# Kernel optimization log

Measured on AMD Instinct MI355X. Metric: run time of the kernel, lower is better.

The kernel has to match this reference:

```python
import jax, jax.numpy as jnp
import numpy as np
from jax import lax

EPS = 1e-5

def conv2d(x, w, pad):
    # x: NCHW, w: OIHW
    return lax.conv_general_dilated(x, w, (1, 1), [(pad, pad), (pad, pad)],
                                    dimension_numbers=('NCHW', 'OIHW', 'NCHW'))

def batchnorm(x, gamma, beta):
    # training-mode BN: batch statistics over N,H,W (biased variance, as torch)
    m = jnp.mean(x, axis=(0, 2, 3), keepdims=True)
    v = jnp.var(x, axis=(0, 2, 3), keepdims=True)
    g = gamma.reshape(1, -1, 1, 1)
    b = beta.reshape(1, -1, 1, 1)
    return (x - m) * jax.lax.rsqrt(v + EPS) * g + b

def setup_inputs() -> dict:
    key = jax.random.key(0)
    ks = jax.random.split(key, 8)
    B, Cin, Cmid, NC, H, W = 4, 2048, 512, 19, 64, 64
    s = lambda fan: (2.0 / fan) ** 0.5
    return {
        'x':  jax.random.normal(ks[0], (B, Cin, H, W), jnp.float32),
        'Wa': jax.random.normal(ks[1], (Cmid, Cin, 3, 3), jnp.float32) * s(Cin * 9),
        'ga': jnp.ones((Cmid,), jnp.float32),
        'ba': jnp.zeros((Cmid,), jnp.float32),
        'Wb': jax.random.normal(ks[2], (Cmid, Cmid, 1, 1), jnp.float32) * s(Cmid),
        'bb': jnp.zeros((Cmid,), jnp.float32),
        'W1': jax.random.normal(ks[3], (Cmid, Cin + Cmid, 3, 3), jnp.float32) * s((Cin + Cmid) * 9),
        'g1': jnp.ones((Cmid,), jnp.float32),
        'b1': jnp.zeros((Cmid,), jnp.float32),
        'W4': jax.random.normal(ks[4], (NC, Cmid, 1, 1), jnp.float32) * s(Cmid),
        'b4': jnp.zeros((NC,), jnp.float32),
    }

def reference(x, Wa, ga, ba, Wb, bb, W1, g1, b1, W4, b4):
    # conva: 3x3 conv (no bias) -> BN -> ReLU
    out = jax.nn.relu(batchnorm(conv2d(x, Wa, 1), ga, ba))
    # convb: 1x1 conv with bias
    out = conv2d(out, Wb, 0) + bb.reshape(1, -1, 1, 1)
    # concat input with projected features along channels
    out = jnp.concatenate([x, out], axis=1)  # [B, Cin+Cmid, H, W]
    # b1 (3x3, no bias) -> b2 BN -> b3 ReLU
    out = jax.nn.relu(batchnorm(conv2d(out, W1, 1), g1, b1))
    # b4: 1x1 classifier conv with bias
    out_final = conv2d(out, W4, 0) + b4.reshape(1, -1, 1, 1)
    return (out, out_final)
```

## Files before the change

kernel.cpp:

```cpp
#include <hip/hip_runtime.h>

typedef unsigned short ushort_t;
typedef unsigned int uint_t;
typedef unsigned long long ulong_t;

typedef __bf16 bf16x8 __attribute__((ext_vector_type(8)));
typedef float f32x4 __attribute__((ext_vector_type(4)));
typedef unsigned short u16x4 __attribute__((ext_vector_type(4)));

#define DEV __device__ __forceinline__
#define SB() __builtin_amdgcn_sched_barrier(0)
#define WAITV(n) asm volatile("s_waitcnt vmcnt(" #n ")" ::: "memory")

DEV ushort_t f2bf(float x) {
  uint_t u = __float_as_uint(x);
  u += 0x7fffu + ((u >> 16) & 1u);
  return (ushort_t)(u >> 16);
}
DEV float bf2f(ushort_t h) { return __uint_as_float(((uint_t)h) << 16); }

DEV void gload16(ulong_t g, const ushort_t* l) {
  __builtin_amdgcn_global_load_lds(
      (__attribute__((address_space(1))) void*)g,
      (__attribute__((address_space(3))) void*)(ushort_t*)l,
      16, 0, 0);
}
DEV int nxt3(int x) { return x == 2 ? 0 : x + 1; }

__global__ void zero_k(float* __restrict__ p, int n) {
  int i = blockIdx.x * 256 + threadIdx.x;
  if (i < n) p[i] = 0.f;
}

__global__ __launch_bounds__(256) void cvt_x_k(const float* __restrict__ X,
                                               ushort_t* __restrict__ P) {
  __shared__ float T[64][65];
  const int t = threadIdx.x;
  const int p0 = blockIdx.x * 64;
  const int c0 = blockIdx.y * 64;
  const int b = p0 >> 12;
  const int pin0 = p0 & 4095;
#pragma unroll
  for (int it = 0; it < 4; ++it) {
    const int cl = it * 16 + (t >> 4);
    const int pl = (t & 15) * 4;
    const f32x4 v = *(const f32x4*)&X[((size_t)(b * 2048 + c0 + cl)) * 4096 + pin0 + pl];
#pragma unroll
    for (int j = 0; j < 4; ++j) T[cl][pl + j] = v[j];
  }
  __syncthreads();
#pragma unroll
  for (int it = 0; it < 4; ++it) {
    const int pl = it * 16 + (t >> 4);
    const int cl = (t & 15) * 4;
    u16x4 h, l;
#pragma unroll
    for (int j = 0; j < 4; ++j) {
      float v = T[cl + j][pl];
      ushort_t hh = f2bf(v);
      h[j] = hh;
      l[j] = f2bf(v - bf2f(hh));
    }
    const int c = c0 + cl;
    const size_t o = (size_t)(p0 + pl) * 4096 + (size_t)((c >> 5) << 6) + (c & 31);
    *(u16x4*)&P[o] = h;
    *(u16x4*)&P[o + 32] = l;
  }
}

__global__ __launch_bounds__(256) void cvt_w3_k(const float* __restrict__ W,
                                                ushort_t* __restrict__ P,
                                                int I, int O) {
  const int t = threadIdx.x;
  const int o = blockIdx.y;
  const int i = blockIdx.x * 256 + t;
  const float* src = W + ((size_t)o * I + i) * 9;
  float v[9];
#pragma unroll
  for (int j = 0; j < 9; ++j) v[j] = src[j];
#pragma unroll
  for (int j = 0; j < 9; ++j) {
    ushort_t h = f2bf(v[j]);
    const size_t d = (size_t)(j * O + o) * (I * 2) + (size_t)((i >> 5) << 6) + (i & 31);
    P[d] = h;
    P[d + 32] = f2bf(v[j] - bf2f(h));
  }
}

__global__ __launch_bounds__(256) void cvt_e_k(const float* __restrict__ W,
                                               ushort_t* __restrict__ P) {
  int i = blockIdx.x * 256 + threadIdx.x;
  float v = W[i];
  ushort_t h = f2bf(v);
  const int o = i >> 9, ic = i & 511;
  const size_t d = (size_t)o * 1024 + (size_t)((ic >> 5) << 6) + (ic & 31);
  P[d] = h;
  P[d + 32] = f2bf(v - bf2f(h));
}

__global__ __launch_bounds__(256) void stats_k(const float* __restrict__ X,
                                               float* __restrict__ S,
                                               float* __restrict__ Q) {
  const int t = threadIdx.x;
  const int r0 = blockIdx.x * 32;
  const int c = t * 2;
  float s0 = 0, s1 = 0, q0 = 0, q1 = 0;
  for (int r = 0; r < 32; ++r) {
    const float2 v = *(const float2*)&X[((size_t)(r0 + r)) * 512 + c];
    s0 += v.x; s1 += v.y;
    q0 += v.x * v.x; q1 += v.y * v.y;
  }
  atomicAdd(&S[c], s0); atomicAdd(&S[c + 1], s1);
  atomicAdd(&Q[c], q0); atomicAdd(&Q[c + 1], q1);
}

__global__ void bnparams_k(const float* __restrict__ S, const float* __restrict__ Q,
                           const float* __restrict__ g, const float* __restrict__ b,
                           float* __restrict__ sc, float* __restrict__ sh) {
  const int t = threadIdx.x;
  const float m = S[t] * (1.0f / 16384.0f);
  const float v = Q[t] * (1.0f / 16384.0f) - m * m;
  const float inv = rsqrtf(v + 1e-5f);
  const float s = g[t] * inv;
  sc[t] = s;
  sh[t] = b[t] - m * s;
}

__global__ __launch_bounds__(256) void bnact_k(const float* __restrict__ X,
                                               const float* __restrict__ sc,
                                               const float* __restrict__ sh,
                                               ushort_t* __restrict__ P) {
  const size_t i0 = ((size_t)blockIdx.x * 256 + threadIdx.x) * 16;
  const int c0 = (int)(i0 & 511);
  const size_t px = i0 >> 9;
#pragma unroll
  for (int q = 0; q < 4; ++q) {
    const f32x4 v = *(const f32x4*)&X[i0 + q * 4];
    const f32x4 s = *(const f32x4*)&sc[c0 + q * 4];
    const f32x4 d = *(const f32x4*)&sh[c0 + q * 4];
    u16x4 h, l;
#pragma unroll
    for (int j = 0; j < 4; ++j) {
      float y = fmaf(v[j], s[j], d[j]);
      y = fmaxf(y, 0.f);
      ushort_t hh = f2bf(y);
      h[j] = hh;
      l[j] = f2bf(y - bf2f(hh));
    }
    const int c = c0 + q * 4;
    const size_t o = px * 1024 + (size_t)((c >> 5) << 6) + (c & 31);
    *(u16x4*)&P[o] = h;
    *(u16x4*)&P[o + 32] = l;
  }
}

__global__ __launch_bounds__(256) void bn_nchw_k(const float* __restrict__ X,
                                                 const float* __restrict__ sc,
                                                 const float* __restrict__ sh,
                                                 float* __restrict__ O) {
  __shared__ float T[64][65];
  const int t = threadIdx.x;
  const int p0 = blockIdx.x * 64;
  const int c0 = blockIdx.y * 64;
  const int b = p0 >> 12, pin0 = p0 & 4095;
#pragma unroll
  for (int it = 0; it < 4; ++it) {
    const int pl = it * 16 + (t >> 4);
    const int cl = (t & 15) * 4;
    const f32x4 v = *(const f32x4*)&X[((size_t)(p0 + pl)) * 512 + c0 + cl];
#pragma unroll
    for (int j = 0; j < 4; ++j) {
      float y = fmaf(v[j], sc[c0 + cl + j], sh[c0 + cl + j]);
      T[pl][cl + j] = fmaxf(y, 0.f);
    }
  }
  __syncthreads();
#pragma unroll
  for (int it = 0; it < 4; ++it) {
    const int cl = it * 16 + (t >> 4);
    const int pl = (t & 15) * 4;
    f32x4 o;
#pragma unroll
    for (int j = 0; j < 4; ++j) o[j] = T[pl + j][cl];
    *(f32x4*)&O[((size_t)(b * 512 + c0 + cl)) * 4096 + pin0 + pl] = o;
  }
}

__global__ __launch_bounds__(256) void conv4_k(const float* __restrict__ X,
                                               const float* __restrict__ sc,
                                               const float* __restrict__ sh,
                                               const float* __restrict__ W4,
                                               const float* __restrict__ B4,
                                               float* __restrict__ O) {
  __shared__ float A[256][69];
  __shared__ float WL[64][19];
  const int t = threadIdx.x;
  const int g0 = blockIdx.x * 256;
  float acc[19];
#pragma unroll
  for (int n = 0; n < 19; ++n) acc[n] = 0.f;
  for (int kc = 0; kc < 8; ++kc) {
    const int k0 = kc * 64;
    __syncthreads();
#pragma unroll
    for (int it = 0; it < 16; ++it) {
      const int rl = it * 16 + (t >> 4);
      const int cl = (t & 15) * 4;
      const f32x4 v = *(const f32x4*)&X[((size_t)(g0 + rl)) * 512 + k0 + cl];
#pragma unroll
      for (int j = 0; j < 4; ++j)
        A[rl][cl + j] = fmaxf(fmaf(v[j], sc[k0 + cl + j], sh[k0 + cl + j]), 0.f);
    }
    for (int e = t; e < 1216; e += 256) {
      int k = e / 19, n = e - k * 19;
      WL[k][n] = W4[(size_t)n * 512 + k0 + k];
    }
    __syncthreads();
#pragma unroll 8
    for (int k = 0; k < 64; ++k) {
      const float a = A[t][k];
#pragma unroll
      for (int n = 0; n < 19; ++n) acc[n] = fmaf(a, WL[k][n], acc[n]);
    }
  }
  const int g = g0 + t;
  const int b = g >> 12, pin = g & 4095;
#pragma unroll
  for (int n = 0; n < 19; ++n)
    O[((size_t)(b * 19 + n)) * 4096 + pin] = acc[n] + B4[n];
}

template <int TAPS, int EPI>
__global__ __launch_bounds__(512, 1) void conv_k(
    const ushort_t* __restrict__ A1, int S1, int CB1,
    const ushort_t* __restrict__ A2, int S2, int CB2,
    const ushort_t* __restrict__ WB, int CBt,
    const ushort_t* __restrict__ zp,
    float* __restrict__ Co, ushort_t* __restrict__ Cp,
    const float* __restrict__ bias) {
  constexpr int RW = (TAPS == 9) ? 6 : 4;
  constexpr int AJ = RW * 4;
  constexpr int AI = (2 * AJ) / 8;
  constexpr int APL = AJ * 1024;
  constexpr int ABUF = 2 * APL;
  constexpr int HO = (TAPS == 9) ? 64 : 0;
  __shared__ ushort_t Alds[49152];
  __shared__ ushort_t Blds[24576];
  const int t = threadIdx.x, lane = t & 63, wid = t >> 6;
  const int wr = wid >> 1, wc = wid & 1;
  const int gid = blockIdx.x, xcd = gid & 7, k_ = gid >> 3;
  const int by = xcd * 8 + (k_ & 7), bx = k_ >> 3;
  const int b = by >> 4, r0 = (by & 15) * 4, bbase = b * 4096;
  const int gsrcA = ((lane & 3) - ((lane >> 3) & 3)) & 3;
  const int NBS = CBt * 64;

  auto stageA = [&](int cb, int bufA) {
#pragma unroll
    for (int i = 0; i < AI; ++i) {
      const int idx = wid * AI + i;
      const int d = idx / AJ, j = idx - d * AJ;
      const int irow = r0 + (j >> 2) - ((TAPS == 9) ? 1 : 0);
      int cbl = cb;
      const ushort_t* base = A1;
      int S = S1;
      if (CB2 > 0 && cbl >= CB1) { base = A2; S = S2; cbl -= CB1; }
      const int gpx = bbase + irow * 64 + (j & 3) * 16 + (lane >> 2);
      const ulong_t el = (ulong_t)gpx * (uint_t)S + (uint_t)(cbl * 64 + d * 32 + gsrcA * 8);
      const bool oob = (unsigned)irow >= 64u;
      const ulong_t src = oob ? (ulong_t)(zp + lane * 8) : (ulong_t)(base + el);
      gload16(src, (const ushort_t*)((const char*)Alds + bufA + (d * AJ + j) * 1024));
    }
  };
  auto stageB = [&](int cb, int tapIdx, int bufB) {
#pragma unroll
    for (int q = 0; q < 2; ++q) {
      const int s = wid * 2 + q, d = s >> 3, nf = s & 7;
      const int cout = bx * 128 + nf * 16 + (lane & 15);
      const ulong_t el = (ulong_t)(tapIdx * 512 + cout) * (uint_t)NBS +
                         (uint_t)(cb * 64 + d * 32 + (lane >> 4) * 8);
      gload16((ulong_t)(WB + el), (const ushort_t*)((const char*)Blds + bufB + s * 1024));
    }
  };

  f32x4 acc[4][4];
#pragma unroll
  for (int i = 0; i < 4; ++i)
#pragma unroll
    for (int j2 = 0; j2 < 4; ++j2) acc[i][j2] = (f32x4){0.f, 0.f, 0.f, 0.f};

  auto compute = [&](int abufB, int bbufB, int ro, int dx) {
    const char* Ab = (const char*)Alds + abufB;
    const char* Bb = (const char*)Blds + bbufB;
    bf16x8 ah[4], al[4], bh[4], bl[4];
#pragma unroll
    for (int i = 0; i < 4; ++i) {
      int px = wr * 64 + i * 16 + (lane & 15) + ro;
      px = px < 0 ? 0 : (px > RW * 64 - 1 ? RW * 64 - 1 : px);
      const int ao = px * 64 + ((((lane >> 4) + (px >> 1)) & 3) * 16);
      ah[i] = *(const bf16x8*)(Ab + ao);
      al[i] = *(const bf16x8*)(Ab + APL + ao);
      bh[i] = *(const bf16x8*)(Bb + (wc * 4 + i) * 1024 + lane * 16);
      bl[i] = *(const bf16x8*)(Bb + 8192 + (wc * 4 + i) * 1024 + lane * 16);
    }
    if (TAPS == 9) {
      if (dx == -1 && (lane & 15) == 0) { bf16x8 z = {}; ah[0] = z; al[0] = z; }
      if (dx == 1 && (lane & 15) == 15) { bf16x8 z = {}; ah[3] = z; al[3] = z; }
    }
    __builtin_amdgcn_s_setprio(1);
#pragma unroll
    for (int mi = 0; mi < 4; ++mi)
#pragma unroll
      for (int ni = 0; ni < 4; ++ni)
        acc[mi][ni] = __builtin_amdgcn_mfma_f32_16x16x32_bf16(ah[mi], bh[ni], acc[mi][ni], 0, 0, 0);
#pragma unroll
    for (int mi = 0; mi < 4; ++mi)
#pragma unroll
      for (int ni = 0; ni < 4; ++ni) {
        acc[mi][ni] = __builtin_amdgcn_mfma_f32_16x16x32_bf16(ah[mi], bl[ni], acc[mi][ni], 0, 0, 0);
        acc[mi][ni] = __builtin_amdgcn_mfma_f32_16x16x32_bf16(al[mi], bh[ni], acc[mi][ni], 0, 0, 0);
      }
    __builtin_amdgcn_s_setprio(0);
  };

  if constexpr (TAPS == 9) {
    int bT = 0;
    stageA(0, 0); SB();
    stageB(0, 0, 0); SB();
    stageB(0, 1, 16384); SB();
    for (int cs = 0; cs < CBt; ++cs) {
      const int abufB = (cs & 1) * ABUF;
#pragma unroll
      for (int tap = 0; tap < 9; ++tap) {
        const int dy = tap / 3 - 1, dx = tap % 3 - 1;
        SB();
        if (tap == 8) { WAITV(8); } else { WAITV(2); }
        SB();
        __builtin_amdgcn_s_barrier();
        SB();
        const int tgt = nxt3(nxt3(bT)) * 16384;
        if (tap < 7) {
          stageB(cs, tap + 2, tgt);
        } else if (tap == 7) {
          stageA(cs + 1, ((cs + 1) & 1) * ABUF);
          stageB(cs + 1, 0, tgt);
        } else {
          stageB(cs + 1, 1, tgt);
        }
        SB();
        compute(abufB, bT * 16384, HO + dy * 64 + dx, dx);
        bT = nxt3(bT);
      }
    }
  } else {
    int rr = 0;
    stageA(0, 0); SB();
    stageB(0, 0, 0); SB();
    stageA(1, ABUF); SB();
    stageB(1, 0, 16384); SB();
    for (int cs = 0; cs < CBt; ++cs) {
      SB();
      WAITV(6);
      SB();
      __builtin_amdgcn_s_barrier();
      SB();
      const int rr2 = nxt3(nxt3(rr));
      stageA(cs + 2, rr2 * ABUF);
      stageB(cs + 2, 0, rr2 * 16384);
      SB();
      compute(rr * ABUF, rr * 16384, 0, 0);
      rr = nxt3(rr);
    }
  }

  const int row0 = by * 256 + wr * 64;
  const int col0 = bx * 128 + wc * 64;
  if (EPI == 0) {
#pragma unroll
    for (int mi = 0; mi < 4; ++mi)
#pragma unroll
      for (int ni = 0; ni < 4; ++ni) {
        const int c = col0 + ni * 16 + (lane & 15);
#pragma unroll
        for (int j2 = 0; j2 < 4; ++j2) {
          const int r = row0 + mi * 16 + (lane >> 4) * 4 + j2;
          Co[(size_t)r * 512 + c] = acc[mi][ni][j2];
        }
      }
  } else {
#pragma unroll
    for (int ni = 0; ni < 4; ++ni) {
      const int c = col0 + ni * 16 + (lane & 15);
      const float bv = bias[c];
      const size_t cg = (size_t)((c >> 5) << 6) + (c & 31);
#pragma unroll
      for (int mi = 0; mi < 4; ++mi)
#pragma unroll
        for (int j2 = 0; j2 < 4; ++j2) {
          const int r = row0 + mi * 16 + (lane >> 4) * 4 + j2;
          const float v = acc[mi][ni][j2] + bv;
          const ushort_t h = f2bf(v);
          Cp[(size_t)r * 1024 + cg] = h;
          Cp[(size_t)r * 1024 + cg + 32] = f2bf(v - bf2f(h));
        }
    }
  }
}

extern "C" void kernel_launch(void* const* d_in, const int* in_sizes, int n_in,
                              void* d_out, int out_size, void* d_ws, size_t ws_size,
                              hipStream_t stream) {
  const float* x  = (const float*)d_in[0];
  const float* Wa = (const float*)d_in[1];
  const float* ga = (const float*)d_in[2];
  const float* ba = (const float*)d_in[3];
  const float* Wb = (const float*)d_in[4];
  const float* bb = (const float*)d_in[5];
  const float* W1 = (const float*)d_in[6];
  const float* g1 = (const float*)d_in[7];
  const float* b1 = (const float*)d_in[8];
  const float* W4 = (const float*)d_in[9];
  const float* b4 = (const float*)d_in[10];
  float* out0 = (float*)d_out;
  float* outF = out0 + (size_t)4 * 512 * 64 * 64;

  char* ws = (char*)d_ws;
  size_t off = 0;
  auto take = [&](size_t bytes) -> char* {
    char* p = ws + off;
    off += (bytes + 255) & ~(size_t)255;
    return p;
  };
  const size_t PAD = 16384;
  ushort_t* zp  = (ushort_t*)take(8192);
  float* sumA = (float*)take(2048);
  float* ssA  = (float*)take(2048);
  float* scA  = (float*)take(2048);
  float* shA  = (float*)take(2048);
  float* sum1 = (float*)take(2048);
  float* ss1  = (float*)take(2048);
  float* sc1  = (float*)take(2048);
  float* sh1  = (float*)take(2048);
  ushort_t* X2  = (ushort_t*)take((size_t)16384 * 4096 * 2 + PAD);
  ushort_t* WA2 = (ushort_t*)take((size_t)9 * 512 * 4096 * 2 + PAD);
  ushort_t* W12 = (ushort_t*)take((size_t)9 * 512 * 5120 * 2 + PAD);
  ushort_t* WBb = (ushort_t*)take((size_t)512 * 1024 * 2 + PAD);
  ushort_t* oA2 = (ushort_t*)take((size_t)16384 * 1024 * 2 + PAD);
  ushort_t* oB2 = (ushort_t*)take((size_t)16384 * 1024 * 2 + PAD);
  float* convaRaw = (float*)take((size_t)16384 * 512 * 4);
  float* conv1Raw = (float*)take((size_t)16384 * 512 * 4);
  if (ws_size < off) return;

  zero_k<<<dim3(24), dim3(256), 0, stream>>>((float*)ws, 6144);
  cvt_x_k<<<dim3(256, 32), dim3(256), 0, stream>>>(x, X2);
  cvt_w3_k<<<dim3(8, 512), dim3(256), 0, stream>>>(Wa, WA2, 2048, 512);
  cvt_w3_k<<<dim3(10, 512), dim3(256), 0, stream>>>(W1, W12, 2560, 512);
  cvt_e_k<<<dim3(1024), dim3(256), 0, stream>>>(Wb, WBb);

  conv_k<9, 0><<<dim3(256), dim3(512), 0, stream>>>(
      X2, 4096, 66, X2, 4096, 0, WA2, 64, zp, convaRaw, nullptr, nullptr);
  stats_k<<<dim3(512), dim3(256), 0, stream>>>(convaRaw, sumA, ssA);
  bnparams_k<<<dim3(1), dim3(512), 0, stream>>>(sumA, ssA, ga, ba, scA, shA);
  bnact_k<<<dim3(2048), dim3(256), 0, stream>>>(convaRaw, scA, shA, oA2);

  conv_k<1, 1><<<dim3(256), dim3(512), 0, stream>>>(
      oA2, 1024, 18, oA2, 1024, 0, WBb, 16, zp, nullptr, oB2, bb);

  conv_k<9, 0><<<dim3(256), dim3(512), 0, stream>>>(
      X2, 4096, 64, oB2, 1024, 16, W12, 80, zp, conv1Raw, nullptr, nullptr);
  stats_k<<<dim3(512), dim3(256), 0, stream>>>(conv1Raw, sum1, ss1);
  bnparams_k<<<dim3(1), dim3(512), 0, stream>>>(sum1, ss1, g1, b1, sc1, sh1);

  bn_nchw_k<<<dim3(256, 8), dim3(256), 0, stream>>>(conv1Raw, sc1, sh1, out0);
  conv4_k<<<dim3(64), dim3(256), 0, stream>>>(conv1Raw, sc1, sh1, W4, b4, outF);
}
```

Before: 2.010 ms.

## Switch conv GEMM to 32x32x16 MFMA with two-tap pipelined staging

Replaces the 16x16x32 bf16 MFMA tiling in the conv kernel with 32x32x16 MFMAs, changing the B-tile LDS layout and swizzle and the epilogue row mapping to match. The 3x3 path now processes two taps per barrier with a four-slot weight ring buffer in a single merged 160KB LDS array. The aim is fewer LDS reads per FLOP and fewer barriers. The full vmcnt drain each step may expose load latency, and launch_bounds is raised to 2 even though the LDS use only allows one block per CU.

```diff
diff --git a/kernel.cpp b/kernel.cpp
--- a/kernel.cpp
+++ b/kernel.cpp
@@ -6,6 +6,7 @@
 
 typedef __bf16 bf16x8 __attribute__((ext_vector_type(8)));
 typedef float f32x4 __attribute__((ext_vector_type(4)));
+typedef float f32x16 __attribute__((ext_vector_type(16)));
 typedef unsigned short u16x4 __attribute__((ext_vector_type(4)));
 
 #define DEV __device__ __forceinline__
@@ -19,10 +20,10 @@
 }
 DEV float bf2f(ushort_t h) { return __uint_as_float(((uint_t)h) << 16); }
 
-DEV void gload16(ulong_t g, const ushort_t* l) {
+DEV void gload16(ulong_t g, const void* l) {
   __builtin_amdgcn_global_load_lds(
       (__attribute__((address_space(1))) void*)g,
-      (__attribute__((address_space(3))) void*)(ushort_t*)l,
+      (__attribute__((address_space(3))) void*)(void*)l,
       16, 0, 0);
 }
 DEV int nxt3(int x) { return x == 2 ? 0 : x + 1; }
@@ -231,7 +232,7 @@
 }
 
 template <int TAPS, int EPI>
-__global__ __launch_bounds__(512, 1) void conv_k(
+__global__ __launch_bounds__(512, 2) void conv_k(
     const ushort_t* __restrict__ A1, int S1, int CB1,
     const ushort_t* __restrict__ A2, int S2, int CB2,
     const ushort_t* __restrict__ WB, int CBt,
@@ -244,14 +245,15 @@
   constexpr int APL = AJ * 1024;
   constexpr int ABUF = 2 * APL;
   constexpr int HO = (TAPS == 9) ? 64 : 0;
-  __shared__ ushort_t Alds[49152];
-  __shared__ ushort_t Blds[24576];
+  __shared__ char lds_all[163840];
+  char* Ald = lds_all;
+  char* Bld = lds_all + 98304;
   const int t = threadIdx.x, lane = t & 63, wid = t >> 6;
   const int wr = wid >> 1, wc = wid & 1;
   const int gid = blockIdx.x, xcd = gid & 7, k_ = gid >> 3;
   const int by = xcd * 8 + (k_ & 7), bx = k_ >> 3;
   const int b = by >> 4, r0 = (by & 15) * 4, bbase = b * 4096;
-  const int gsrcA = ((lane & 3) - ((lane >> 3) & 3)) & 3;
+  const int gsrc = ((lane & 3) - ((lane >> 3) & 3)) & 3;
   const int NBS = CBt * 64;
 
   auto stageA = [&](int cb, int bufA) {
@@ -265,90 +267,124 @@
       int S = S1;
       if (CB2 > 0 && cbl >= CB1) { base = A2; S = S2; cbl -= CB1; }
       const int gpx = bbase + irow * 64 + (j & 3) * 16 + (lane >> 2);
-      const ulong_t el = (ulong_t)gpx * (uint_t)S + (uint_t)(cbl * 64 + d * 32 + gsrcA * 8);
+      const ulong_t el = (ulong_t)gpx * (uint_t)S + (uint_t)(cbl * 64 + d * 32 + gsrc * 8);
       const bool oob = (unsigned)irow >= 64u;
       const ulong_t src = oob ? (ulong_t)(zp + lane * 8) : (ulong_t)(base + el);
-      gload16(src, (const ushort_t*)((const char*)Alds + bufA + (d * AJ + j) * 1024));
+      gload16(src, Ald + bufA + (d * AJ + j) * 1024);
     }
   };
   auto stageB = [&](int cb, int tapIdx, int bufB) {
 #pragma unroll
     for (int q = 0; q < 2; ++q) {
-      const int s = wid * 2 + q, d = s >> 3, nf = s & 7;
-      const int cout = bx * 128 + nf * 16 + (lane & 15);
-      const ulong_t el = (ulong_t)(tapIdx * 512 + cout) * (uint_t)NBS +
-                         (uint_t)(cb * 64 + d * 32 + (lane >> 4) * 8);
-      gload16((ulong_t)(WB + el), (const ushort_t*)((const char*)Blds + bufB + s * 1024));
+      const int s = wid * 2 + q;
+      const int d = s >> 3, r = s & 7, nb = r >> 1, h = r & 1;
+      const int co = bx * 128 + nb * 32 + h * 16 + (lane >> 2);
+      const ulong_t el = (ulong_t)(tapIdx * 512 + co) * (uint_t)NBS +
+                         (uint_t)(cb * 64 + d * 32 + gsrc * 8);
+      gload16((ulong_t)(WB + el), Bld + bufB + s * 1024);
     }
   };
 
-  f32x4 acc[4][4];
-#pragma unroll
-  for (int i = 0; i < 4; ++i)
-#pragma unroll
-    for (int j2 = 0; j2 < 4; ++j2) acc[i][j2] = (f32x4){0.f, 0.f, 0.f, 0.f};
+  f32x16 acc[2][2];
+#pragma unroll
+  for (int i = 0; i < 2; ++i)
+#pragma unroll
+    for (int j2 = 0; j2 < 2; ++j2) acc[i][j2] = (f32x16){0.f};
+
+  const int pxl = lane & 31;
+  const int khalf = lane >> 5;
+  const int rotB = (pxl >> 1) & 3;
+  int boff[2][2];
+#pragma unroll
+  for (int ni = 0; ni < 2; ++ni)
+#pragma unroll
+    for (int kk = 0; kk < 2; ++kk) {
+      const int pos = (kk * 2 + khalf + rotB) & 3;
+      boff[ni][kk] = (wc * 2 + ni) * 2048 + pxl * 64 + pos * 16;
+    }
 
   auto compute = [&](int abufB, int bbufB, int ro, int dx) {
-    const char* Ab = (const char*)Alds + abufB;
-    const char* Bb = (const char*)Blds + bbufB;
-    bf16x8 ah[4], al[4], bh[4], bl[4];
-#pragma unroll
-    for (int i = 0; i < 4; ++i) {
-      int px = wr * 64 + i * 16 + (lane & 15) + ro;
-      px = px < 0 ? 0 : (px > RW * 64 - 1 ? RW * 64 - 1 : px);
-      const int ao = px * 64 + ((((lane >> 4) + (px >> 1)) & 3) * 16);
-      ah[i] = *(const bf16x8*)(Ab + ao);
-      al[i] = *(const bf16x8*)(Ab + APL + ao);
-      bh[i] = *(const bf16x8*)(Bb + (wc * 4 + i) * 1024 + lane * 16);
-      bl[i] = *(const bf16x8*)(Bb + 8192 + (wc * 4 + i) * 1024 + lane * 16);
-    }
+    const char* Ab = Ald + abufB;
+    const char* Bb = Bld + bbufB;
+    bf16x8 a[2][2][2], bf[2][2][2];
+#pragma unroll
+    for (int mi = 0; mi < 2; ++mi)
+#pragma unroll
+      for (int kk = 0; kk < 2; ++kk) {
+        int px = wr * 64 + mi * 32 + pxl + ro;
+        px = px < 0 ? 0 : (px > RW * 64 - 1 ? RW * 64 - 1 : px);
+        const int pos = (kk * 2 + khalf + (px >> 1)) & 3;
+        const int ao = px * 64 + pos * 16;
+        a[mi][kk][0] = *(const bf16x8*)(Ab + ao);
+        a[mi][kk][1] = *(const bf16x8*)(Ab + APL + ao);
+      }
+#pragma unroll
+    for (int ni = 0; ni < 2; ++ni)
+#pragma unroll
+      for (int kk = 0; kk < 2; ++kk) {
+        bf[ni][kk][0] = *(const bf16x8*)(Bb + boff[ni][kk]);
+        bf[ni][kk][1] = *(const bf16x8*)(Bb + 8192 + boff[ni][kk]);
+      }
     if (TAPS == 9) {
-      if (dx == -1 && (lane & 15) == 0) { bf16x8 z = {}; ah[0] = z; al[0] = z; }
-      if (dx == 1 && (lane & 15) == 15) { bf16x8 z = {}; ah[3] = z; al[3] = z; }
+      if (dx == -1 && pxl == 0) {
+        bf16x8 z = {};
+        a[0][0][0] = z; a[0][0][1] = z; a[0][1][0] = z; a[0][1][1] = z;
+      }
+      if (dx == 1 && pxl == 31) {
+        bf16x8 z = {};
+        a[1][0][0] = z; a[1][0][1] = z; a[1][1][0] = z; a[1][1][1] = z;
+      }
     }
     __builtin_amdgcn_s_setprio(1);
 #pragma unroll
-    for (int mi = 0; mi < 4; ++mi)
-#pragma unroll
-      for (int ni = 0; ni < 4; ++ni)
-        acc[mi][ni] = __builtin_amdgcn_mfma_f32_16x16x32_bf16(ah[mi], bh[ni], acc[mi][ni], 0, 0, 0);
-#pragma unroll
-    for (int mi = 0; mi < 4; ++mi)
-#pragma unroll
-      for (int ni = 0; ni < 4; ++ni) {
-        acc[mi][ni] = __builtin_amdgcn_mfma_f32_16x16x32_bf16(ah[mi], bl[ni], acc[mi][ni], 0, 0, 0);
-        acc[mi][ni] = __builtin_amdgcn_mfma_f32_16x16x32_bf16(al[mi], bh[ni], acc[mi][ni], 0, 0, 0);
-      }
+    for (int kk = 0; kk < 2; ++kk)
+#pragma unroll
+      for (int mi = 0; mi < 2; ++mi)
+#pragma unroll
+        for (int ni = 0; ni < 2; ++ni) {
+          acc[mi][ni] = __builtin_amdgcn_mfma_f32_32x32x16_bf16(
+              a[mi][kk][0], bf[ni][kk][0], acc[mi][ni], 0, 0, 0);
+          acc[mi][ni] = __builtin_amdgcn_mfma_f32_32x32x16_bf16(
+              a[mi][kk][0], bf[ni][kk][1], acc[mi][ni], 0, 0, 0);
+          acc[mi][ni] = __builtin_amdgcn_mfma_f32_32x32x16_bf16(
+              a[mi][kk][1], bf[ni][kk][0], acc[mi][ni], 0, 0, 0);
+        }
     __builtin_amdgcn_s_setprio(0);
   };
 
   if constexpr (TAPS == 9) {
-    int bT = 0;
-    stageA(0, 0); SB();
-    stageB(0, 0, 0); SB();
-    stageB(0, 1, 16384); SB();
-    for (int cs = 0; cs < CBt; ++cs) {
-      const int abufB = (cs & 1) * ABUF;
-#pragma unroll
-      for (int tap = 0; tap < 9; ++tap) {
-        const int dy = tap / 3 - 1, dx = tap % 3 - 1;
-        SB();
-        if (tap == 8) { WAITV(8); } else { WAITV(2); }
-        SB();
-        __builtin_amdgcn_s_barrier();
-        SB();
-        const int tgt = nxt3(nxt3(bT)) * 16384;
-        if (tap < 7) {
-          stageB(cs, tap + 2, tgt);
-        } else if (tap == 7) {
-          stageA(cs + 1, ((cs + 1) & 1) * ABUF);
-          stageB(cs + 1, 0, tgt);
-        } else {
-          stageB(cs + 1, 1, tgt);
-        }
-        SB();
-        compute(abufB, bT * 16384, HO + dy * 64 + dx, dx);
-        bT = nxt3(bT);
+    const int NT = CBt * 9;
+    stageA(0, 0);
+    stageB(0, 0, 0);
+    stageB(0, 1, 16384);
+    SB();
+    for (int T = 0; T < NT; T += 2) {
+      WAITV(0);
+      SB();
+      __builtin_amdgcn_s_barrier();
+      SB();
+      const int T2 = T + 2, T3 = T + 3;
+      if (T2 < NT) {
+        const int cs2 = T2 / 9, tp2 = T2 - cs2 * 9;
+        if (tp2 == 0) stageA(cs2, (cs2 & 1) * ABUF);
+        stageB(cs2, tp2, (T2 & 3) * 16384);
+      }
+      if (T3 < NT) {
+        const int cs3 = T3 / 9, tp3 = T3 - cs3 * 9;
+        if (tp3 == 0) stageA(cs3, (cs3 & 1) * ABUF);
+        stageB(cs3, tp3, (T3 & 3) * 16384);
+      }
+      SB();
+      {
+        const int cs = T / 9, tap = T - cs * 9;
+        const int dy = tap / 3 - 1, dx = tap - (tap / 3) * 3 - 1;
+        compute((cs & 1) * ABUF, (T & 3) * 16384, HO + dy * 64 + dx, dx);
+      }
+      {
+        const int T1 = T + 1;
+        const int cs = T1 / 9, tap = T1 - cs * 9;
+        const int dy = tap / 3 - 1, dx = tap - (tap / 3) * 3 - 1;
+        compute((cs & 1) * ABUF, (T1 & 3) * 16384, HO + dy * 64 + dx, dx);
       }
     }
   } else {
@@ -374,30 +410,31 @@
 
   const int row0 = by * 256 + wr * 64;
   const int col0 = bx * 128 + wc * 64;
+  const int rb = 4 * khalf;
   if (EPI == 0) {
 #pragma unroll
-    for (int mi = 0; mi < 4; ++mi)
-#pragma unroll
-      for (int ni = 0; ni < 4; ++ni) {
-        const int c = col0 + ni * 16 + (lane & 15);
-#pragma unroll
-        for (int j2 = 0; j2 < 4; ++j2) {
-          const int r = row0 + mi * 16 + (lane >> 4) * 4 + j2;
-          Co[(size_t)r * 512 + c] = acc[mi][ni][j2];
+    for (int mi = 0; mi < 2; ++mi)
+#pragma unroll
+      for (int ni = 0; ni < 2; ++ni) {
+        const int c = col0 + ni * 32 + pxl;
+#pragma unroll
+        for (int rg = 0; rg < 16; ++rg) {
+          const int r = row0 + mi * 32 + (rg & 3) + 8 * (rg >> 2) + rb;
+          Co[(size_t)r * 512 + c] = acc[mi][ni][rg];
         }
       }
   } else {
 #pragma unroll
-    for (int ni = 0; ni < 4; ++ni) {
-      const int c = col0 + ni * 16 + (lane & 15);
+    for (int ni = 0; ni < 2; ++ni) {
+      const int c = col0 + ni * 32 + pxl;
       const float bv = bias[c];
       const size_t cg = (size_t)((c >> 5) << 6) + (c & 31);
 #pragma unroll
-      for (int mi = 0; mi < 4; ++mi)
-#pragma unroll
-        for (int j2 = 0; j2 < 4; ++j2) {
-          const int r = row0 + mi * 16 + (lane >> 4) * 4 + j2;
-          const float v = acc[mi][ni][j2] + bv;
+      for (int mi = 0; mi < 2; ++mi)
+#pragma unroll
+        for (int rg = 0; rg < 16; ++rg) {
+          const int r = row0 + mi * 32 + (rg & 3) + 8 * (rg >> 2) + rb;
+          const float v = acc[mi][ni][rg] + bv;
           const ushort_t h = f2bf(v);
           Cp[(size_t)r * 1024 + cg] = h;
           Cp[(size_t)r * 1024 + cg + 32] = f2bf(v - bf2f(h));
@@ -457,7 +494,7 @@
   cvt_e_k<<<dim3(1024), dim3(256), 0, stream>>>(Wb, WBb);
 
   conv_k<9, 0><<<dim3(256), dim3(512), 0, stream>>>(
-      X2, 4096, 66, X2, 4096, 0, WA2, 64, zp, convaRaw, nullptr, nullptr);
+      X2, 4096, 64, X2, 4096, 0, WA2, 64, zp, convaRaw, nullptr, nullptr);
   stats_k<<<dim3(512), dim3(256), 0, stream>>>(convaRaw, sumA, ssA);
   bnparams_k<<<dim3(1), dim3(512), 0, stream>>>(sumA, ssA, ga, ba, scA, shA);
   bnact_k<<<dim3(2048), dim3(256), 0, stream>>>(convaRaw, scA, shA, oA2);
```

New measurement: 1.979 ms. Within noise of the previous version (-1.5%).
